# Kernel tuning notes

Measured on AMD Instinct MI355X. Metric: run time of the kernel, lower is better.

## Reference

```python
import jax, jax.numpy as jnp
import numpy as np

DIM = 512
NUM_HEADS = 16
RANK = 4
HEAD_DIM = DIM // NUM_HEADS
SCALE = HEAD_DIM ** -0.5
B_, N, NW = 2048, 49, 64


def setup_inputs() -> dict:
    key = jax.random.key(0)
    ks = jax.random.split(key, 9)
    x = jax.random.normal(ks[0], (B_, N, DIM), dtype=jnp.float32)
    mask = jax.random.normal(ks[1], (NW, N, N), dtype=jnp.float32)
    # qkv base linear (torch Linear stores weight [out,in])
    W_qkv = jax.random.normal(ks[2], (3 * DIM, DIM), dtype=jnp.float32) * (DIM ** -0.5)
    b_qkv = jax.random.normal(ks[3], (3 * DIM,), dtype=jnp.float32) * 0.02
    # LoRA down [rank, dim], up [3*dim, rank] (zero-init in module; use small random for non-trivial math)
    A_down = jax.random.normal(ks[4], (RANK, DIM), dtype=jnp.float32) * 0.02
    B_up = jax.random.normal(ks[5], (3 * DIM, RANK), dtype=jnp.float32) * 0.02
    W_proj = jax.random.normal(ks[6], (DIM, DIM), dtype=jnp.float32) * (DIM ** -0.5)
    b_proj = jax.random.normal(ks[7], (DIM,), dtype=jnp.float32) * 0.02
    return {"x": x, "mask": mask, "W_qkv": W_qkv, "b_qkv": b_qkv,
            "A_down": A_down, "B_up": B_up, "W_proj": W_proj, "b_proj": b_proj}


def reference(x, mask, W_qkv, b_qkv, A_down, B_up, W_proj, b_proj):
    Bw, n, C = x.shape
    H, hd = NUM_HEADS, HEAD_DIM
    # LoRA-augmented QKV projection: base linear + up(down(x))
    qkv = x @ W_qkv.T + b_qkv + (x @ A_down.T) @ B_up.T          # [B_, N, 3C]
    qkv = qkv.reshape(Bw, n, 3, H, hd)
    q = qkv[:, :, 0].transpose(0, 2, 1, 3)                        # [B_, H, N, hd]
    k = qkv[:, :, 1].transpose(0, 2, 1, 3)
    v = qkv[:, :, 2].transpose(0, 2, 1, 3)
    attn = jnp.einsum('bhnd,bhmd->bhnm', q, k) * SCALE            # [B_, H, N, N]
    nW = mask.shape[0]
    attn = attn.reshape(Bw // nW, nW, H, n, n) + mask[None, :, None]
    attn = attn.reshape(Bw, H, n, n)
    attn = jax.nn.softmax(attn, axis=-1)
    out = jnp.einsum('bhnm,bhmd->bhnd', attn, v)                  # [B_, H, N, hd]
    out = out.transpose(0, 2, 1, 3).reshape(Bw, n, C)
    return out @ W_proj.T + b_proj
```

## Files before the change

### kernel.cpp

```cpp
#include <hip/hip_runtime.h>
#include <stdint.h>

typedef __attribute__((ext_vector_type(4))) float f32x4;
typedef __attribute__((ext_vector_type(8))) __bf16 bf16x8;
typedef __attribute__((ext_vector_type(4))) unsigned int u32x4;
typedef __attribute__((ext_vector_type(4))) unsigned short u16x4;

#define TOK 49
#define NHEAD 16
#define HDIM 32
#define CDIM 512
#define NB 2048
#define MTOT (NB * TOK)
#define ATT_SCALE 0.17677669529663687f

__device__ __forceinline__ unsigned short f2bf(float f) {
  uint32_t u = __builtin_bit_cast(uint32_t, f);
  u += 0x7FFFu + ((u >> 16) & 1u);
  return (unsigned short)(u >> 16);
}

__device__ __forceinline__ void gl_lds16(const void* g, const void* lds) {
  __builtin_amdgcn_global_load_lds(
      (__attribute__((address_space(1))) void*)(uintptr_t)g,
      (__attribute__((address_space(3))) void*)(uint32_t)(uintptr_t)lds,
      16, 0, 0);
}

__device__ __forceinline__ f32x4 mfma16(bf16x8 a, bf16x8 b, f32x4 c) {
  return __builtin_amdgcn_mfma_f32_16x16x32_bf16(a, b, c, 0, 0, 0);
}

__global__ __launch_bounds__(256) void k_prep_weff(
    const float* __restrict__ Wqkv, const float* __restrict__ Bup,
    const float* __restrict__ Adown, unsigned short* __restrict__ weff) {
  int idx = blockIdx.x * 256 + threadIdx.x;
  if (idx >= 3 * CDIM * CDIM) return;
  int o = idx >> 9, i = idx & 511;
  float v = Wqkv[idx];
#pragma unroll
  for (int r = 0; r < 4; r++) v += Bup[o * 4 + r] * Adown[r * 512 + i];
  weff[idx] = f2bf(v);
}

__global__ __launch_bounds__(256) void k_conv4(
    const float* __restrict__ src, unsigned short* __restrict__ dst, int n4) {
  for (int i = blockIdx.x * blockDim.x + threadIdx.x; i < n4;
       i += gridDim.x * blockDim.x) {
    f32x4 v = *(const f32x4*)(src + (size_t)i * 4);
    u16x4 o;
    o[0] = f2bf(v[0]); o[1] = f2bf(v[1]); o[2] = f2bf(v[2]); o[3] = f2bf(v[3]);
    *(u16x4*)(dst + (size_t)i * 4) = o;
  }
}

template <int NT, bool SPLIT>
__global__ __launch_bounds__(512, 1) void k_gemm256(
    const unsigned short* __restrict__ A, const unsigned short* __restrict__ Bw,
    const float* __restrict__ bias,
    unsigned short* __restrict__ qo, unsigned short* __restrict__ ko,
    unsigned short* __restrict__ vo, float* __restrict__ fo) {
  __shared__ __attribute__((aligned(16))) unsigned short lA[2][256 * 64];
  __shared__ __attribute__((aligned(16))) unsigned short lB[2][256 * 64];
  const int t = threadIdx.x;
  const int l = t & 63;
  const int l15 = l & 15, lq = l >> 4;
  const int w = t >> 6;
  const int wr = w >> 2, wc = w & 3;
  const int bid = blockIdx.x;
  const int lb = (bid & 7) * ((int)gridDim.x >> 3) + (bid >> 3);
  const int mt = lb / NT, nt = lb % NT;
  const size_t m0 = (size_t)mt * 256;
  const int n0 = nt * 256;

  auto stage = [&](int kt, int bb) {
#pragma unroll
    for (int q = 0; q < 4; ++q) {
      const int li = q * 512 + t;
      const int row = li >> 3, sl = li & 7;
      gl_lds16(A + (m0 + row) * CDIM + kt * 64 + ((sl ^ (row & 7)) << 3),
               &lA[bb][li * 8]);
    }
#pragma unroll
    for (int q = 0; q < 4; ++q) {
      const int li = q * 512 + t;
      const int row = li >> 3, sl = li & 7;
      gl_lds16(Bw + (size_t)(n0 + row) * CDIM + kt * 64 + ((sl ^ (row & 7)) << 3),
               &lB[bb][li * 8]);
    }
  };

  f32x4 acc[8][4] = {};
  stage(0, 0);
  for (int kt = 0; kt < 8; ++kt) {
    const int cur = kt & 1;
    if (kt < 7) {
      stage(kt + 1, cur ^ 1);
      asm volatile("s_waitcnt vmcnt(8)" ::: "memory");
    } else {
      asm volatile("s_waitcnt vmcnt(0)" ::: "memory");
    }
    __builtin_amdgcn_s_barrier();
    asm volatile("" ::: "memory");
    const unsigned short* bufA = &lA[cur][0];
    const unsigned short* bufB = &lB[cur][0];

    bf16x8 bfr[4][2];
#pragma unroll
    for (int c = 0; c < 4; ++c) {
      const int r = wc * 64 + c * 16 + l15;
#pragma unroll
      for (int h = 0; h < 2; ++h)
        bfr[c][h] = __builtin_bit_cast(
            bf16x8,
            *(const u32x4*)&bufB[r * 64 + (((lq + h * 4) ^ (r & 7)) << 3)]);
    }

    auto loadA = [&](bf16x8(&dst)[2][2], int p) {
#pragma unroll
      for (int rr = 0; rr < 2; ++rr) {
        const int r = wr * 128 + (p * 2 + rr) * 16 + l15;
#pragma unroll
        for (int h = 0; h < 2; ++h)
          dst[rr][h] = __builtin_bit_cast(
              bf16x8,
              *(const u32x4*)&bufA[r * 64 + (((lq + h * 4) ^ (r & 7)) << 3)]);
      }
    };

    bf16x8 afA[2][2], afB[2][2];
    loadA(afA, 0);
#pragma unroll
    for (int p = 0; p < 4; ++p) {
      bf16x8(&cur_)[2][2] = (p & 1) ? afB : afA;
      bf16x8(&nxt_)[2][2] = (p & 1) ? afA : afB;
      if (p < 3) loadA(nxt_, p + 1);
      __builtin_amdgcn_s_setprio(1);
#pragma unroll
      for (int rr = 0; rr < 2; ++rr) {
#pragma unroll
        for (int c = 0; c < 4; ++c) {
          acc[p * 2 + rr][c] = mfma16(cur_[rr][0], bfr[c][0], acc[p * 2 + rr][c]);
          acc[p * 2 + rr][c] = mfma16(cur_[rr][1], bfr[c][1], acc[p * 2 + rr][c]);
        }
      }
      __builtin_amdgcn_s_setprio(0);
    }
    asm volatile("" ::: "memory");
    __builtin_amdgcn_s_barrier();
  }

#pragma unroll
  for (int J = 0; J < 4; ++J) {
    const int colb = n0 + wc * 64 + J * 16 + l15;
    const float bv = bias[colb];
    if constexpr (SPLIT) {
      const int which = colb >> 9;
      const int hh = (colb >> 5) & 15;
      const int d = colb & 31;
      unsigned short* dst = which == 0 ? qo : (which == 1 ? ko : vo);
#pragma unroll
      for (int I = 0; I < 8; ++I) {
#pragma unroll
        for (int r = 0; r < 4; ++r) {
          uint32_t m = (uint32_t)(m0 + wr * 128 + I * 16 + lq * 4 + r);
          uint32_t bw_ = m / 49u;
          uint32_t nn = m - bw_ * 49u;
          dst[((size_t)(bw_ * 16u + hh) * 49u + nn) * 32u + d] =
              f2bf(acc[I][J][r] + bv);
        }
      }
    } else {
#pragma unroll
      for (int I = 0; I < 8; ++I) {
#pragma unroll
        for (int r = 0; r < 4; ++r) {
          size_t m = m0 + wr * 128 + I * 16 + lq * 4 + r;
          fo[m * CDIM + colb] = acc[I][J][r] + bv;
        }
      }
    }
  }
}

__global__ __launch_bounds__(256) void k_attn(
    const unsigned short* __restrict__ qb, const unsigned short* __restrict__ kb,
    const unsigned short* __restrict__ vb, const float* __restrict__ mask,
    unsigned short* __restrict__ ao) {
  __shared__ __attribute__((aligned(16))) unsigned short sP[4][64 * 64];
  __shared__ __attribute__((aligned(16))) unsigned short sV[4][32 * 64];
  const int t = threadIdx.x;
  const int l = t & 63, w = t >> 6;
  const int l15 = l & 15, lq = l >> 4;
  const int pair = blockIdx.x * 4 + w;
  const int b = pair >> 4, h = pair & 15;
  const size_t base = (size_t)pair * (TOK * HDIM);
  unsigned short* P = sP[w];
  unsigned short* Vt = sV[w];

  bf16x8 qf[4], kf[4];
#pragma unroll
  for (int i = 0; i < 4; i++)
    qf[i] = __builtin_bit_cast(
        bf16x8, *(const u32x4*)(qb + base + (size_t)(i * 16 + l15) * 32 + lq * 8));
#pragma unroll
  for (int i = 0; i < 4; i++)
    kf[i] = __builtin_bit_cast(
        bf16x8, *(const u32x4*)(kb + base + (size_t)(i * 16 + l15) * 32 + lq * 8));
  u32x4 vr[4];
#pragma unroll
  for (int j = 0; j < 4; j++)
    vr[j] = *(const u32x4*)(vb + base + (size_t)l * 32 + j * 8);

  f32x4 s[4][4];
  __builtin_amdgcn_s_setprio(1);
#pragma unroll
  for (int i = 0; i < 4; i++) {
#pragma unroll
    for (int j = 0; j < 4; j++) s[i][j] = mfma16(qf[i], kf[j], (f32x4)0.0f);
  }
  __builtin_amdgcn_s_setprio(0);

  const bool vok = (l < TOK);
  const int tsl = ((l >> 3) & 7);
  const int tlo = l & 7;
#pragma unroll
  for (int j = 0; j < 4; j++) {
#pragma unroll
    for (int c = 0; c < 4; c++) {
      uint32_t u = vr[j][c];
      int d0 = j * 8 + c * 2;
      Vt[(d0 + 0) * 64 + ((tsl ^ ((d0 + 0) & 7)) << 3) + tlo] =
          vok ? (unsigned short)(u & 0xFFFFu) : (unsigned short)0;
      Vt[(d0 + 1) * 64 + ((tsl ^ ((d0 + 1) & 7)) << 3) + tlo] =
          vok ? (unsigned short)(u >> 16) : (unsigned short)0;
    }
  }

  const float* mrow = mask + (size_t)(b & 63) * (TOK * TOK);
#pragma unroll
  for (int i = 0; i < 4; i++) {
#pragma unroll
    for (int r = 0; r < 4; r++) {
      int row = i * 16 + lq * 4 + r;
#pragma unroll
      for (int j = 0; j < 4; j++) {
        int col = j * 16 + l15;
        float xv = s[i][j][r] * ATT_SCALE;
        if (col < TOK) {
          if (row < TOK) xv += mrow[row * TOK + col];
        } else {
          xv = -1e30f;
        }
        s[i][j][r] = xv;
      }
    }
  }

  float rinv[4][4];
#pragma unroll
  for (int i = 0; i < 4; i++) {
#pragma unroll
    for (int r = 0; r < 4; r++) {
      float m = fmaxf(fmaxf(s[i][0][r], s[i][1][r]), fmaxf(s[i][2][r], s[i][3][r]));
      m = fmaxf(m, __shfl_xor(m, 1));
      m = fmaxf(m, __shfl_xor(m, 2));
      m = fmaxf(m, __shfl_xor(m, 4));
      m = fmaxf(m, __shfl_xor(m, 8));
      float sum = 0.f;
      int row = i * 16 + lq * 4 + r;
#pragma unroll
      for (int j = 0; j < 4; j++) {
        float p = __expf(s[i][j][r] - m);
        sum += p;
        P[row * 64 + (((j * 2 + (l15 >> 3)) ^ (row & 7)) << 3) + (l15 & 7)] =
            f2bf(p);
      }
      sum += __shfl_xor(sum, 1);
      sum += __shfl_xor(sum, 2);
      sum += __shfl_xor(sum, 4);
      sum += __shfl_xor(sum, 8);
      rinv[i][r] = 1.0f / sum;
    }
  }

  asm volatile("s_waitcnt lgkmcnt(0)" ::: "memory");
  __builtin_amdgcn_sched_barrier(0);

  f32x4 o[4][2] = {};
#pragma unroll
  for (int ks = 0; ks < 2; ks++) {
    bf16x8 pa[4], vf[2];
#pragma unroll
    for (int i = 0; i < 4; i++)
      pa[i] = __builtin_bit_cast(
          bf16x8,
          *(const u32x4*)&P[(i * 16 + l15) * 64 + (((lq + ks * 4) ^ (l15 & 7)) << 3)]);
#pragma unroll
    for (int j = 0; j < 2; j++)
      vf[j] = __builtin_bit_cast(
          bf16x8,
          *(const u32x4*)&Vt[(j * 16 + l15) * 64 + (((lq + ks * 4) ^ (l15 & 7)) << 3)]);
    __builtin_amdgcn_s_setprio(1);
#pragma unroll
    for (int i = 0; i < 4; i++) {
#pragma unroll
      for (int j = 0; j < 2; j++) o[i][j] = mfma16(pa[i], vf[j], o[i][j]);
    }
    __builtin_amdgcn_s_setprio(0);
  }

#pragma unroll
  for (int i = 0; i < 4; i++) {
#pragma unroll
    for (int r = 0; r < 4; r++) {
      int row = i * 16 + lq * 4 + r;
      if (row < TOK) {
        float inv = rinv[i][r];
        size_t obase = ((size_t)b * TOK + row) * CDIM + h * HDIM;
#pragma unroll
        for (int j = 0; j < 2; j++)
          ao[obase + j * 16 + l15] = f2bf(o[i][j][r] * inv);
      }
    }
  }
}

extern "C" void kernel_launch(void* const* d_in, const int* in_sizes, int n_in,
                              void* d_out, int out_size, void* d_ws,
                              size_t ws_size, hipStream_t stream) {
  const float* x = (const float*)d_in[0];
  const float* mask = (const float*)d_in[1];
  const float* Wqkv = (const float*)d_in[2];
  const float* bqkv = (const float*)d_in[3];
  const float* Adown = (const float*)d_in[4];
  const float* Bup = (const float*)d_in[5];
  const float* Wproj = (const float*)d_in[6];
  const float* bproj = (const float*)d_in[7];
  float* out = (float*)d_out;
  char* ws = (char*)d_ws;

  size_t off = 0;
  auto alloc = [&](size_t bytes) {
    size_t o = off;
    off += (bytes + 255) & ~(size_t)255;
    return o;
  };
  const size_t qkv_elems = (size_t)NB * NHEAD * TOK * HDIM;
  unsigned short* weff = (unsigned short*)(ws + alloc((size_t)3 * CDIM * CDIM * 2));
  unsigned short* wpb = (unsigned short*)(ws + alloc((size_t)CDIM * CDIM * 2));
  unsigned short* qb = (unsigned short*)(ws + alloc(qkv_elems * 2 + 4096));
  unsigned short* kb = (unsigned short*)(ws + alloc(qkv_elems * 2 + 4096));
  unsigned short* vb = (unsigned short*)(ws + alloc(qkv_elems * 2 + 4096));
  unsigned short* xb = (unsigned short*)(ws + alloc((size_t)MTOT * CDIM * 2));
  unsigned short* ao = xb;

  k_prep_weff<<<(3 * CDIM * CDIM + 255) / 256, 256, 0, stream>>>(Wqkv, Bup,
                                                                 Adown, weff);
  k_conv4<<<256, 256, 0, stream>>>(Wproj, wpb, CDIM * CDIM / 4);
  k_conv4<<<2048, 256, 0, stream>>>(x, xb, MTOT * CDIM / 4);
  k_gemm256<6, true><<<(MTOT / 256) * 6, 512, 0, stream>>>(
      xb, weff, bqkv, qb, kb, vb, nullptr);
  k_attn<<<NB * NHEAD / 4, 256, 0, stream>>>(qb, kb, vb, mask, ao);
  k_gemm256<2, false><<<(MTOT / 256) * 2, 512, 0, stream>>>(
      ao, wpb, bproj, nullptr, nullptr, nullptr, out);
}
```

Before: 606.3 us.

## Restructure GEMM main loop into barrier-synced phases interleaving loads and MFMA

Splits the global-to-LDS staging into separate A and B halves and issues them during the first two of four per-k-tile compute phases instead of all at the loop top. Each phase loads a quarter of the A and B fragments, synchronises with barriers, then runs 16 MFMAs. The goal is to overlap global loads with matrix math more evenly and reduce register pressure from holding all B fragments. The trade-off is two barriers per phase, eight per k-tile, which adds synchronisation overhead.

```diff
diff --git a/kernel.cpp b/kernel.cpp
--- a/kernel.cpp
+++ b/kernel.cpp
@@ -73,7 +73,7 @@
   const size_t m0 = (size_t)mt * 256;
   const int n0 = nt * 256;
 
-  auto stage = [&](int kt, int bb) {
+  auto stageA = [&](int kt, int bb) {
 #pragma unroll
     for (int q = 0; q < 4; ++q) {
       const int li = q * 512 + t;
@@ -81,6 +81,8 @@
       gl_lds16(A + (m0 + row) * CDIM + kt * 64 + ((sl ^ (row & 7)) << 3),
                &lA[bb][li * 8]);
     }
+  };
+  auto stageB = [&](int kt, int bb) {
 #pragma unroll
     for (int q = 0; q < 4; ++q) {
       const int li = q * 512 + t;
@@ -91,63 +93,54 @@
   };
 
   f32x4 acc[8][4] = {};
-  stage(0, 0);
+  stageA(0, 0);
+  stageB(0, 0);
+  asm volatile("s_waitcnt vmcnt(0)" ::: "memory");
+  __builtin_amdgcn_s_barrier();
+
   for (int kt = 0; kt < 8; ++kt) {
-    const int cur = kt & 1;
-    if (kt < 7) {
-      stage(kt + 1, cur ^ 1);
-      asm volatile("s_waitcnt vmcnt(8)" ::: "memory");
-    } else {
-      asm volatile("s_waitcnt vmcnt(0)" ::: "memory");
-    }
-    __builtin_amdgcn_s_barrier();
-    asm volatile("" ::: "memory");
+    const int cur = kt & 1, nb = cur ^ 1;
     const unsigned short* bufA = &lA[cur][0];
     const unsigned short* bufB = &lB[cur][0];
-
-    bf16x8 bfr[4][2];
-#pragma unroll
-    for (int c = 0; c < 4; ++c) {
-      const int r = wc * 64 + c * 16 + l15;
-#pragma unroll
-      for (int h = 0; h < 2; ++h)
-        bfr[c][h] = __builtin_bit_cast(
+#pragma unroll
+    for (int p = 0; p < 4; ++p) {
+      const int qi = p & 1;
+      const int kh = p >> 1;
+      bf16x8 af[4], bfv[4];
+#pragma unroll
+      for (int rr = 0; rr < 4; ++rr) {
+        const int r = wr * 128 + qi * 64 + rr * 16 + l15;
+        af[rr] = __builtin_bit_cast(
             bf16x8,
-            *(const u32x4*)&bufB[r * 64 + (((lq + h * 4) ^ (r & 7)) << 3)]);
-    }
-
-    auto loadA = [&](bf16x8(&dst)[2][2], int p) {
-#pragma unroll
-      for (int rr = 0; rr < 2; ++rr) {
-        const int r = wr * 128 + (p * 2 + rr) * 16 + l15;
-#pragma unroll
-        for (int h = 0; h < 2; ++h)
-          dst[rr][h] = __builtin_bit_cast(
-              bf16x8,
-              *(const u32x4*)&bufA[r * 64 + (((lq + h * 4) ^ (r & 7)) << 3)]);
-      }
-    };
-
-    bf16x8 afA[2][2], afB[2][2];
-    loadA(afA, 0);
-#pragma unroll
-    for (int p = 0; p < 4; ++p) {
-      bf16x8(&cur_)[2][2] = (p & 1) ? afB : afA;
-      bf16x8(&nxt_)[2][2] = (p & 1) ? afA : afB;
-      if (p < 3) loadA(nxt_, p + 1);
+            *(const u32x4*)&bufA[r * 64 + (((lq + kh * 4) ^ (r & 7)) << 3)]);
+      }
+#pragma unroll
+      for (int c = 0; c < 4; ++c) {
+        const int r = wc * 64 + c * 16 + l15;
+        bfv[c] = __builtin_bit_cast(
+            bf16x8,
+            *(const u32x4*)&bufB[r * 64 + (((lq + kh * 4) ^ (r & 7)) << 3)]);
+      }
+      if (p == 0 && kt < 7) stageA(kt + 1, nb);
+      if (p == 1 && kt < 7) stageB(kt + 1, nb);
+      asm volatile("" ::: "memory");
+      __builtin_amdgcn_s_barrier();
+      asm volatile("s_waitcnt lgkmcnt(0)" ::: "memory");
+      __builtin_amdgcn_sched_barrier(0);
       __builtin_amdgcn_s_setprio(1);
 #pragma unroll
-      for (int rr = 0; rr < 2; ++rr) {
-#pragma unroll
-        for (int c = 0; c < 4; ++c) {
-          acc[p * 2 + rr][c] = mfma16(cur_[rr][0], bfr[c][0], acc[p * 2 + rr][c]);
-          acc[p * 2 + rr][c] = mfma16(cur_[rr][1], bfr[c][1], acc[p * 2 + rr][c]);
-        }
+      for (int rr = 0; rr < 4; ++rr) {
+#pragma unroll
+        for (int c = 0; c < 4; ++c)
+          acc[qi * 4 + rr][c] = mfma16(af[rr], bfv[c], acc[qi * 4 + rr][c]);
       }
       __builtin_amdgcn_s_setprio(0);
-    }
-    asm volatile("" ::: "memory");
-    __builtin_amdgcn_s_barrier();
+      if (p == 3) {
+        asm volatile("s_waitcnt vmcnt(0)" ::: "memory");
+      }
+      asm volatile("" ::: "memory");
+      __builtin_amdgcn_s_barrier();
+    }
   }
 
 #pragma unroll
```

After: 609.8 us. No clear change (+0.6%).
